# Performance work log

Measured on AMD Instinct MI355X. Metric: run time of the kernel, lower is better.

## Reference

```python
import math
import jax, jax.numpy as jnp
import numpy as np

B, T, C, H = 4, 2048, 1024, 16
D = C // H  # head dim = 64


def setup_inputs() -> dict:
    key = jax.random.key(0)
    ks = jax.random.split(key, 5)
    s = 1.0 / math.sqrt(C)
    return {
        "x": jax.random.normal(ks[0], (B, T, C), jnp.float32),
        "w_qkv": jax.random.normal(ks[1], (C, 3 * C), jnp.float32) * s,
        "b_qkv": jax.random.normal(ks[2], (3 * C,), jnp.float32) * 0.02,
        "w_out": jax.random.normal(ks[3], (C, C), jnp.float32) * s,
        "b_out": jax.random.normal(ks[4], (C,), jnp.float32) * 0.02,
    }


def reference(x, w_qkv, b_qkv, w_out, b_out):
    # qkv projection: (B,T,C) @ (C,3C) -> split into Q,K,V
    qkv = x @ w_qkv + b_qkv
    q, k, v = jnp.split(qkv, 3, axis=-1)
    # reshape to (B,H,T,D)
    q = q.reshape(B, T, H, D).transpose(0, 2, 1, 3)
    k = k.reshape(B, T, H, D).transpose(0, 2, 1, 3)
    v = v.reshape(B, T, H, D).transpose(0, 2, 1, 3)
    # scaled scores with causal mask
    scores = jnp.einsum("bhqd,bhkd->bhqk", q, k) * (1.0 / math.sqrt(D))
    causal = jnp.tril(jnp.ones((T, T), dtype=bool))
    scores = jnp.where(causal[None, None], scores, -jnp.inf)
    attn = jax.nn.softmax(scores, axis=-1)  # dropout_rate=0 (eval)
    out = jnp.einsum("bhqk,bhkd->bhqd", attn, v)
    out = out.transpose(0, 2, 1, 3).reshape(B, T, C)
    return out @ w_out + b_out
```

## Files before the change

### kernel.cpp

```cpp
#include <hip/hip_runtime.h>
#include <cstdint>
#include <cstddef>

typedef _Float16 h8_t __attribute__((ext_vector_type(8)));
typedef _Float16 h4_t __attribute__((ext_vector_type(4)));
typedef float f32x4 __attribute__((ext_vector_type(4)));
typedef float f32x16 __attribute__((ext_vector_type(16)));
typedef unsigned u32x4 __attribute__((ext_vector_type(4)));

#define MFMA_16x16x32_F16(a, b, c) __builtin_amdgcn_mfma_f32_16x16x32_f16(a, b, c, 0, 0, 0)
#define MFMA_32x32x16_F16(a, b, c) __builtin_amdgcn_mfma_f32_32x32x16_f16(a, b, c, 0, 0, 0)

__device__ inline void gload_lds16(const void* g, void* l) {
  __builtin_amdgcn_global_load_lds((const __attribute__((address_space(1))) void*)g,
                                   (__attribute__((address_space(3))) void*)l, 16, 0, 0);
}

#define CFENCE asm volatile("" ::: "memory")
#define RAW_BAR() do { CFENCE; __builtin_amdgcn_s_barrier(); CFENCE; } while (0)

__global__ void cvt_f16_kernel(const float* __restrict__ in, _Float16* __restrict__ out, int n4) {
  int i = blockIdx.x * 256 + threadIdx.x;
  if (i >= n4) return;
  float4 v = reinterpret_cast<const float4*>(in)[i];
  h4_t h;
  h[0] = (_Float16)v.x; h[1] = (_Float16)v.y; h[2] = (_Float16)v.z; h[3] = (_Float16)v.w;
  reinterpret_cast<h4_t*>(out)[i] = h;
}

__global__ void transpose_cvt_kernel(const float* __restrict__ in, _Float16* __restrict__ out,
                                     int R, int Cc) {
  __shared__ float tile[32][33];
  int tx = threadIdx.x & 31;
  int ty = threadIdx.x >> 5;
  int c0 = blockIdx.x * 32;
  int r0 = blockIdx.y * 32;
#pragma unroll
  for (int i = 0; i < 4; ++i)
    tile[ty + i * 8][tx] = in[(size_t)(r0 + ty + i * 8) * Cc + (c0 + tx)];
  __syncthreads();
#pragma unroll
  for (int i = 0; i < 4; ++i)
    out[(size_t)(c0 + ty + i * 8) * R + (r0 + tx)] = (_Float16)tile[tx][ty + i * 8];
}

template <int EPI>
__global__ __launch_bounds__(256, 3) void gemm_bt_kernel(
    const _Float16* __restrict__ A, const _Float16* __restrict__ Bt,
    const float* __restrict__ bias, _Float16* __restrict__ outQ,
    _Float16* __restrict__ outK, _Float16* __restrict__ outV,
    float* __restrict__ outF, int NB) {
  __shared__ _Float16 Al[3][4096];
  __shared__ _Float16 Bl[3][4096];
  const int tid = threadIdx.x;
  const int lane = tid & 63;
  const int w = tid >> 6;
  const int bm = blockIdx.x / NB;
  const int bn = blockIdx.x % NB;
  const int wm = w & 1, wn = w >> 1;
  const int m0 = bm * 128, n0 = bn * 128;

  f32x4 acc[4][4];
#pragma unroll
  for (int m = 0; m < 4; ++m)
#pragma unroll
    for (int n = 0; n < 4; ++n) acc[m][n] = (f32x4){0.f, 0.f, 0.f, 0.f};

  const int seg0 = w * 2, seg1 = w * 2 + 1;
  const int r0s = seg0 * 16 + (lane >> 2);
  const int r1s = seg1 * 16 + (lane >> 2);
  const int c0s = ((lane & 3) ^ ((r0s >> 1) & 3)) * 8;
  const int c1s = ((lane & 3) ^ ((r1s >> 1) & 3)) * 8;
  const _Float16* aS0 = A + (size_t)(m0 + r0s) * 1024 + c0s;
  const _Float16* aS1 = A + (size_t)(m0 + r1s) * 1024 + c1s;
  const _Float16* bS0 = Bt + (size_t)(n0 + r0s) * 1024 + c0s;
  const _Float16* bS1 = Bt + (size_t)(n0 + r1s) * 1024 + c1s;
  const int d0 = seg0 * 512 + lane * 8;
  const int d1 = seg1 * 512 + lane * 8;

  auto stage = [&](int buf, int kt) {
    const int k0 = kt * 32;
    gload_lds16(aS0 + k0, &Al[buf][d0]);
    gload_lds16(bS0 + k0, &Bl[buf][d0]);
    gload_lds16(aS1 + k0, &Al[buf][d1]);
    gload_lds16(bS1 + k0, &Bl[buf][d1]);
  };

  int offA[4], offB[4];
#pragma unroll
  for (int i = 0; i < 4; ++i) {
    const int rowA = wm * 64 + i * 16 + (lane & 15);
    offA[i] = rowA * 32 + (((lane >> 4) ^ ((rowA >> 1) & 3)) * 8);
    const int rowB = wn * 64 + i * 16 + (lane & 15);
    offB[i] = rowB * 32 + (((lane >> 4) ^ ((rowB >> 1) & 3)) * 8);
  }

  stage(0, 0);
  stage(1, 1);
  asm volatile("s_waitcnt vmcnt(4)" ::: "memory");
  RAW_BAR();

  int cur = 0;
#pragma unroll 1
  for (int t = 0; t < 32; ++t) {
    int nb = cur + 2; if (nb >= 3) nb -= 3;
    if (t + 2 < 32) stage(nb, t + 2);
    const _Float16* Ab = &Al[cur][0];
    const _Float16* Bb = &Bl[cur][0];
    h8_t af[4], bf[4];
#pragma unroll
    for (int i = 0; i < 4; ++i) af[i] = *(const h8_t*)&Ab[offA[i]];
#pragma unroll
    for (int j = 0; j < 4; ++j) bf[j] = *(const h8_t*)&Bb[offB[j]];
#pragma unroll
    for (int i = 0; i < 4; ++i)
#pragma unroll
      for (int j = 0; j < 4; ++j)
        acc[i][j] = MFMA_16x16x32_F16(af[i], bf[j], acc[i][j]);
    if (t < 31) {
      if (t + 2 < 32) asm volatile("s_waitcnt vmcnt(4)" ::: "memory");
      else asm volatile("s_waitcnt vmcnt(0)" ::: "memory");
      RAW_BAR();
    }
    ++cur; if (cur == 3) cur = 0;
  }

  const int gm0 = bm * 128 + wm * 64;
  const int gn0 = bn * 128 + wn * 64;
#pragma unroll
  for (int i = 0; i < 4; ++i) {
#pragma unroll
    for (int j = 0; j < 4; ++j) {
      const int gn = gn0 + j * 16 + (lane & 15);
      const int tm0 = gm0 + i * 16 + (lane >> 4) * 4;
      const float bv = bias[gn];
      if (EPI == 0) {
        const int which = gn >> 10;
        const int nn = gn & 1023;
        const int h = nn >> 6, d = nn & 63;
        const int t0 = tm0 & 2047, b = tm0 >> 11;
        const int bh = b * 16 + h;
        if (which == 2) {
          h4_t pack;
#pragma unroll
          for (int r = 0; r < 4; ++r) pack[r] = (_Float16)(acc[i][j][r] + bv);
          *reinterpret_cast<h4_t*>(&outV[((size_t)bh * 64 + d) * 2048 + t0]) = pack;
        } else {
          _Float16* dst = (which == 0) ? outQ : outK;
          const float scale = (which == 0) ? 0.18033688011112042f : 1.0f;
#pragma unroll
          for (int r = 0; r < 4; ++r)
            dst[((size_t)bh * 2048 + t0 + r) * 64 + d] = (_Float16)((acc[i][j][r] + bv) * scale);
        }
      } else {
#pragma unroll
        for (int r = 0; r < 4; ++r)
          outF[(size_t)(tm0 + r) * 1024 + gn] = acc[i][j][r] + bv;
      }
    }
  }
}

__device__ inline void stage_kv(const _Float16* __restrict__ Kbh, const _Float16* __restrict__ Vbh,
                                int kt, _Float16* Kd, _Float16* Vd, int w, int lane) {
  const _Float16* Kg = Kbh + (size_t)kt * 64 * 64;
  const _Float16* Vg = Vbh + kt * 64;
#pragma unroll
  for (int c = 0; c < 2; ++c) {
    const int idx = (2 * w + c) * 64 + lane;
    const int row = idx >> 3;
    const int chs = (idx & 7) ^ (row & 7);
    gload_lds16(Kg + row * 64 + chs * 8, Kd + idx * 8);
    gload_lds16(Vg + (size_t)row * 2048 + chs * 8, Vd + idx * 8);
  }
}

__device__ inline void pack_pfrag(const float* e, h8_t* out) {
  unsigned u[8];
#pragma unroll
  for (int i = 0; i < 8; ++i) {
    auto hv = __builtin_amdgcn_cvt_pkrtz(e[2 * i], e[2 * i + 1]);
    u[i] = __builtin_bit_cast(unsigned, hv);
  }
  auto r02 = __builtin_amdgcn_permlane32_swap(u[0], u[2], false, false);
  auto r13 = __builtin_amdgcn_permlane32_swap(u[1], u[3], false, false);
  auto r46 = __builtin_amdgcn_permlane32_swap(u[4], u[6], false, false);
  auto r57 = __builtin_amdgcn_permlane32_swap(u[5], u[7], false, false);
  u32x4 w0 = {(unsigned)r02[0], (unsigned)r13[0], (unsigned)r02[1], (unsigned)r13[1]};
  u32x4 w1 = {(unsigned)r46[0], (unsigned)r57[0], (unsigned)r46[1], (unsigned)r57[1]};
  out[0] = __builtin_bit_cast(h8_t, w0);
  out[1] = __builtin_bit_cast(h8_t, w1);
}

__global__ __launch_bounds__(256, 2) void attn_kernel(
    const _Float16* __restrict__ Q, const _Float16* __restrict__ K,
    const _Float16* __restrict__ Vt, _Float16* __restrict__ O) {
  __shared__ _Float16 Kl[2][64 * 64];
  __shared__ _Float16 Vl[2][64 * 64];
  const int tid = threadIdx.x;
  const int lane = tid & 63;
  const int w = tid >> 6;
  const int hi = lane >> 5;
  const int l31 = lane & 31;
  const int bh = blockIdx.x >> 3;
  const int pr = blockIdx.x & 7;
  const int b = bh >> 4, h = bh & 15;
  const _Float16* Kbh = K + (size_t)bh * 2048 * 64;
  const _Float16* Vbh = Vt + (size_t)bh * 64 * 2048;

#pragma unroll
  for (int gi = 0; gi < 2; ++gi) {
    const int g = gi ? (15 - pr) : pr;
    const int nt = 2 * g + 2;
    const int qbase = g * 128 + w * 32;
    const int qrow = qbase + l31;

    h8_t qf[4];
    const _Float16* Qp = Q + ((size_t)bh * 2048 + qrow) * 64 + hi * 8;
#pragma unroll
    for (int ds = 0; ds < 4; ++ds)
      qf[ds] = *reinterpret_cast<const h8_t*>(Qp + ds * 16);

    f32x16 oa[2] = {};
    float m = -1e30f, lsum = 0.f;

    stage_kv(Kbh, Vbh, 0, &Kl[0][0], &Vl[0][0], w, lane);
    __syncthreads();

    for (int kt = 0; kt < nt; ++kt) {
      const int cur = kt & 1;
      if (kt + 1 < nt)
        stage_kv(Kbh, Vbh, kt + 1, &Kl[cur ^ 1][0], &Vl[cur ^ 1][0], w, lane);

      if (kt * 64 <= qbase + 31) {
        const char* Kb = (const char*)&Kl[cur][0];
        const char* Vb = (const char*)&Vl[cur][0];
        f32x16 s0 = {}, s1 = {};
#pragma unroll
        for (int ds = 0; ds < 4; ++ds) {
          const int bc = ds * 32 + hi * 16;
          h8_t kf0 = *(const h8_t*)(Kb + l31 * 128 + (bc ^ ((l31 & 7) << 4)));
          h8_t kf1 = *(const h8_t*)(Kb + (32 + l31) * 128 + (bc ^ ((l31 & 7) << 4)));
          s0 = MFMA_32x32x16_F16(kf0, qf[ds], s0);
          s1 = MFMA_32x32x16_F16(kf1, qf[ds], s1);
        }
        if (kt >= 2 * g) {
#pragma unroll
          for (int r = 0; r < 16; ++r) {
            const int kr = kt * 64 + (r & 3) + 8 * (r >> 2) + 4 * hi;
            if (kr > qrow) s0[r] = -1e30f;
            if (kr + 32 > qrow) s1[r] = -1e30f;
          }
        }
        float t[16];
#pragma unroll
        for (int r = 0; r < 16; ++r) t[r] = fmaxf(s0[r], s1[r]);
#pragma unroll
        for (int st = 8; st >= 1; st >>= 1)
#pragma unroll
          for (int r = 0; r < st; ++r) t[r] = fmaxf(t[r], t[r + st]);
        const float pmax = fmaxf(t[0], __shfl_xor(t[0], 32));
        const float mnew = fmaxf(m, pmax);
        if (__any(mnew > m + 8.f)) {
          const float al = __builtin_amdgcn_exp2f(m - mnew);
          lsum *= al;
#pragma unroll
          for (int r = 0; r < 16; ++r) { oa[0][r] *= al; oa[1][r] *= al; }
          m = mnew;
        }
        float e0[16], e1[16];
#pragma unroll
        for (int r = 0; r < 16; ++r) {
          e0[r] = __builtin_amdgcn_exp2f(s0[r] - m);
          e1[r] = __builtin_amdgcn_exp2f(s1[r] - m);
        }
        float ps = 0.f;
#pragma unroll
        for (int r = 0; r < 16; ++r) ps += e0[r] + e1[r];
        ps += __shfl_xor(ps, 32);
        lsum += ps;
        h8_t pf[4];
        pack_pfrag(e0, pf + 0);
        pack_pfrag(e1, pf + 2);
#pragma unroll
        for (int dt = 0; dt < 2; ++dt) {
#pragma unroll
          for (int kg = 0; kg < 4; ++kg) {
            const int row = dt * 32 + l31;
            const int bc = kg * 32 + hi * 16;
            h8_t vf = *(const h8_t*)(Vb + row * 128 + (bc ^ ((row & 7) << 4)));
            oa[dt] = MFMA_32x32x16_F16(vf, pf[kg], oa[dt]);
          }
        }
      }
      __syncthreads();
    }

    const float inv = __builtin_amdgcn_rcpf(lsum);
    _Float16* Op = O + ((size_t)b * 2048 + qrow) * 1024 + h * 64;
#pragma unroll
    for (int dt = 0; dt < 2; ++dt) {
#pragma unroll
      for (int rg = 0; rg < 4; ++rg) {
        h4_t pk4;
#pragma unroll
        for (int i = 0; i < 4; ++i) pk4[i] = (_Float16)(oa[dt][rg * 4 + i] * inv);
        *reinterpret_cast<h4_t*>(Op + dt * 32 + rg * 8 + hi * 4) = pk4;
      }
    }
  }
}

extern "C" void kernel_launch(void* const* d_in, const int* in_sizes, int n_in,
                              void* d_out, int out_size, void* d_ws, size_t ws_size,
                              hipStream_t stream) {
  (void)in_sizes; (void)n_in; (void)out_size; (void)ws_size;
  const float* x = (const float*)d_in[0];
  const float* w_qkv = (const float*)d_in[1];
  const float* b_qkv = (const float*)d_in[2];
  const float* w_out = (const float*)d_in[3];
  const float* b_out = (const float*)d_in[4];
  float* out = (float*)d_out;

  char* ws = (char*)d_ws;
  size_t off = 0;
  auto alloc = [&](size_t bytes) {
    void* p = ws + off;
    off += (bytes + 255) & ~(size_t)255;
    return p;
  };
  _Float16* x16 = (_Float16*)alloc((size_t)8192 * 1024 * 2);
  _Float16* wqkvT = (_Float16*)alloc((size_t)3072 * 1024 * 2);
  _Float16* woutT = (_Float16*)alloc((size_t)1024 * 1024 * 2);
  _Float16* Qh = (_Float16*)alloc((size_t)64 * 2048 * 64 * 2);
  _Float16* Kh = (_Float16*)alloc((size_t)64 * 2048 * 64 * 2);
  _Float16* Vth = (_Float16*)alloc((size_t)64 * 64 * 2048 * 2);
  _Float16* Oh = (_Float16*)alloc((size_t)8192 * 1024 * 2);

  cvt_f16_kernel<<<8192, 256, 0, stream>>>(x, x16, 8192 * 1024 / 4);
  transpose_cvt_kernel<<<dim3(3072 / 32, 1024 / 32), 256, 0, stream>>>(w_qkv, wqkvT, 1024, 3072);
  transpose_cvt_kernel<<<dim3(1024 / 32, 1024 / 32), 256, 0, stream>>>(w_out, woutT, 1024, 1024);
  gemm_bt_kernel<0><<<64 * 24, 256, 0, stream>>>(x16, wqkvT, b_qkv, Qh, Kh, Vth, nullptr, 24);
  attn_kernel<<<64 * 8, 256, 0, stream>>>(Qh, Kh, Vth, Oh);
  gemm_bt_kernel<1><<<64 * 8, 256, 0, stream>>>(Oh, woutT, b_out, nullptr, nullptr, nullptr, out, 8);
}
```

Baseline: 184.2 us.

## Use dedicated 256x384-tile QKV GEMM kernel with 512 threads and split staging

Replaces the templated 128x128 GEMM for the QKV projection with a dedicated kernel that has 8 waves, 256x384 block tiles and 128x96 per-wave tiles. The grid becomes 256 blocks, one per CU, and each k-step interleaves A and B staging with two halves of MFMA work, raising priority around the MFMA bursts. The larger tile is meant to raise arithmetic intensity and cut global and LDS reloads. In exchange it uses much more LDS and registers (192 accumulator floats per lane) and leaves a single wave of blocks with no tail balancing. The output projection keeps the old kernel, now split out as a non-templated version.

```diff
diff --git a/kernel.cpp b/kernel.cpp
--- a/kernel.cpp
+++ b/kernel.cpp
@@ -44,12 +44,136 @@
     out[(size_t)(c0 + ty + i * 8) * R + (r0 + tx)] = (_Float16)tile[tx][ty + i * 8];
 }
 
-template <int EPI>
-__global__ __launch_bounds__(256, 3) void gemm_bt_kernel(
+__global__ __launch_bounds__(512, 2) void gemm_qkv_kernel(
     const _Float16* __restrict__ A, const _Float16* __restrict__ Bt,
     const float* __restrict__ bias, _Float16* __restrict__ outQ,
-    _Float16* __restrict__ outK, _Float16* __restrict__ outV,
-    float* __restrict__ outF, int NB) {
+    _Float16* __restrict__ outK, _Float16* __restrict__ outV) {
+  __shared__ _Float16 Al[3][8192];
+  __shared__ _Float16 Bl[3][12288];
+
+  const int tid = threadIdx.x;
+  const int lane = tid & 63;
+  const int w = tid >> 6;
+  const int wm = w >> 2, wn = w & 3;
+  const int bm = blockIdx.x >> 3;
+  const int bn = blockIdx.x & 7;
+  const int m0 = bm * 256;
+  const int n0 = bn * 384;
+
+  f32x4 acc[8][6];
+#pragma unroll
+  for (int i = 0; i < 8; ++i)
+#pragma unroll
+    for (int j = 0; j < 6; ++j) acc[i][j] = (f32x4){0.f, 0.f, 0.f, 0.f};
+
+  const int fg0 = tid >> 6;
+  const int sl = tid & 63;
+  const int srow = fg0 * 16 + (sl & 15);
+  const int scol = (sl >> 4) * 8;
+  const _Float16* aS = A + (size_t)(m0 + srow) * 1024 + scol;
+  const _Float16* bS = Bt + (size_t)(n0 + srow) * 1024 + scol;
+  const int sdst = tid * 8;
+
+  auto stageA = [&](int buf, int kt) {
+    const int k0 = kt * 32;
+    gload_lds16(aS + k0, &Al[buf][sdst]);
+    gload_lds16(aS + 131072 + k0, &Al[buf][sdst + 4096]);
+  };
+  auto stageB = [&](int buf, int kt) {
+    const int k0 = kt * 32;
+    gload_lds16(bS + k0, &Bl[buf][sdst]);
+    gload_lds16(bS + 131072 + k0, &Bl[buf][sdst + 4096]);
+    gload_lds16(bS + 262144 + k0, &Bl[buf][sdst + 8192]);
+  };
+
+  const int offA0 = (wm * 8 * 64 + lane) * 8;
+  const int offB0 = (wn * 6 * 64 + lane) * 8;
+
+  stageA(0, 0); stageB(0, 0);
+  stageA(1, 1); stageB(1, 1);
+  asm volatile("s_waitcnt vmcnt(5)" ::: "memory");
+  RAW_BAR();
+
+  int cur = 0;
+#pragma unroll 1
+  for (int t = 0; t < 32; ++t) {
+    int nb = cur + 2; if (nb >= 3) nb -= 3;
+    const bool st = (t + 2) < 32;
+    const _Float16* Ab = &Al[cur][0];
+    const _Float16* Bb = &Bl[cur][0];
+    h8_t af[4], bf[6];
+
+#pragma unroll
+    for (int mf = 0; mf < 4; ++mf) af[mf] = *(const h8_t*)&Ab[offA0 + mf * 512];
+#pragma unroll
+    for (int nf = 0; nf < 6; ++nf) bf[nf] = *(const h8_t*)&Bb[offB0 + nf * 512];
+    if (st) stageA(nb, t + 2);
+    RAW_BAR();
+    asm volatile("s_waitcnt lgkmcnt(0)" ::: "memory");
+    __builtin_amdgcn_sched_barrier(0);
+    __builtin_amdgcn_s_setprio(1);
+#pragma unroll
+    for (int mf = 0; mf < 4; ++mf)
+#pragma unroll
+      for (int nf = 0; nf < 6; ++nf)
+        acc[mf][nf] = MFMA_16x16x32_F16(af[mf], bf[nf], acc[mf][nf]);
+    __builtin_amdgcn_s_setprio(0);
+    RAW_BAR();
+
+#pragma unroll
+    for (int mf = 0; mf < 4; ++mf) af[mf] = *(const h8_t*)&Ab[offA0 + (4 + mf) * 512];
+    if (st) stageB(nb, t + 2);
+    RAW_BAR();
+    asm volatile("s_waitcnt lgkmcnt(0)" ::: "memory");
+    __builtin_amdgcn_sched_barrier(0);
+    __builtin_amdgcn_s_setprio(1);
+#pragma unroll
+    for (int mf = 0; mf < 4; ++mf)
+#pragma unroll
+      for (int nf = 0; nf < 6; ++nf)
+        acc[4 + mf][nf] = MFMA_16x16x32_F16(af[mf], bf[nf], acc[4 + mf][nf]);
+    __builtin_amdgcn_s_setprio(0);
+    if (t < 31) {
+      if (st) asm volatile("s_waitcnt vmcnt(5)" ::: "memory");
+      else asm volatile("s_waitcnt vmcnt(0)" ::: "memory");
+      RAW_BAR();
+    }
+    ++cur; if (cur == 3) cur = 0;
+  }
+
+  const int gm0 = m0 + wm * 128;
+  const int gn0 = n0 + wn * 96;
+#pragma unroll
+  for (int mf = 0; mf < 8; ++mf) {
+#pragma unroll
+    for (int nf = 0; nf < 6; ++nf) {
+      const int gn = gn0 + nf * 16 + (lane & 15);
+      const int tm0 = gm0 + mf * 16 + (lane >> 4) * 4;
+      const float bv = bias[gn];
+      const int which = gn >> 10;
+      const int nn = gn & 1023;
+      const int h = nn >> 6, d = nn & 63;
+      const int t0 = tm0 & 2047, b = tm0 >> 11;
+      const int bh = b * 16 + h;
+      if (which == 2) {
+        h4_t pack;
+#pragma unroll
+        for (int r = 0; r < 4; ++r) pack[r] = (_Float16)(acc[mf][nf][r] + bv);
+        *reinterpret_cast<h4_t*>(&outV[((size_t)bh * 64 + d) * 2048 + t0]) = pack;
+      } else {
+        _Float16* dst = (which == 0) ? outQ : outK;
+        const float scale = (which == 0) ? 0.18033688011112042f : 1.0f;
+#pragma unroll
+        for (int r = 0; r < 4; ++r)
+          dst[((size_t)bh * 2048 + t0 + r) * 64 + d] = (_Float16)((acc[mf][nf][r] + bv) * scale);
+      }
+    }
+  }
+}
+
+__global__ __launch_bounds__(256, 3) void gemm_out_kernel(
+    const _Float16* __restrict__ A, const _Float16* __restrict__ Bt,
+    const float* __restrict__ bias, float* __restrict__ outF, int NB) {
   __shared__ _Float16 Al[3][4096];
   __shared__ _Float16 Bl[3][4096];
   const int tid = threadIdx.x;
@@ -134,29 +258,9 @@
       const int gn = gn0 + j * 16 + (lane & 15);
       const int tm0 = gm0 + i * 16 + (lane >> 4) * 4;
       const float bv = bias[gn];
-      if (EPI == 0) {
-        const int which = gn >> 10;
-        const int nn = gn & 1023;
-        const int h = nn >> 6, d = nn & 63;
-        const int t0 = tm0 & 2047, b = tm0 >> 11;
-        const int bh = b * 16 + h;
-        if (which == 2) {
-          h4_t pack;
-#pragma unroll
-          for (int r = 0; r < 4; ++r) pack[r] = (_Float16)(acc[i][j][r] + bv);
-          *reinterpret_cast<h4_t*>(&outV[((size_t)bh * 64 + d) * 2048 + t0]) = pack;
-        } else {
-          _Float16* dst = (which == 0) ? outQ : outK;
-          const float scale = (which == 0) ? 0.18033688011112042f : 1.0f;
-#pragma unroll
-          for (int r = 0; r < 4; ++r)
-            dst[((size_t)bh * 2048 + t0 + r) * 64 + d] = (_Float16)((acc[i][j][r] + bv) * scale);
-        }
-      } else {
-#pragma unroll
-        for (int r = 0; r < 4; ++r)
-          outF[(size_t)(tm0 + r) * 1024 + gn] = acc[i][j][r] + bv;
-      }
+#pragma unroll
+      for (int r = 0; r < 4; ++r)
+        outF[(size_t)(tm0 + r) * 1024 + gn] = acc[i][j][r] + bv;
     }
   }
 }
@@ -340,7 +444,7 @@
   cvt_f16_kernel<<<8192, 256, 0, stream>>>(x, x16, 8192 * 1024 / 4);
   transpose_cvt_kernel<<<dim3(3072 / 32, 1024 / 32), 256, 0, stream>>>(w_qkv, wqkvT, 1024, 3072);
   transpose_cvt_kernel<<<dim3(1024 / 32, 1024 / 32), 256, 0, stream>>>(w_out, woutT, 1024, 1024);
-  gemm_bt_kernel<0><<<64 * 24, 256, 0, stream>>>(x16, wqkvT, b_qkv, Qh, Kh, Vth, nullptr, 24);
+  gemm_qkv_kernel<<<256, 512, 0, stream>>>(x16, wqkvT, b_qkv, Qh, Kh, Vth);
   attn_kernel<<<64 * 8, 256, 0, stream>>>(Qh, Kh, Vth, Oh);
-  gemm_bt_kernel<1><<<64 * 8, 256, 0, stream>>>(Oh, woutT, b_out, nullptr, nullptr, nullptr, out, 8);
-}
+  gemm_out_kernel<<<64 * 8, 256, 0, stream>>>(Oh, woutT, b_out, out, 8);
+}
```

Result: faster. 179.1 us (-2.8%).
